# Kernel tuning notes

Hardware: AMD Instinct MI355X
Metric: run time of the kernel (lower is better)

## Reference

```python
import jax, jax.numpy as jnp
import numpy as np

N_NODES = 50000
N_EDGES = 800000
FEAT_DIM = 1024
EMBED_DIM = 128


def setup_inputs() -> dict:
    key = jax.random.key(0)
    k_x, k_w, k_r, k_c, k_v = jax.random.split(key, 5)
    x = jax.random.normal(k_x, (N_NODES, FEAT_DIM), dtype=jnp.float32)
    # xavier-uniform equivalent for weight [embed_dim, feat_dim]
    limit = float(np.sqrt(6.0 / (EMBED_DIM + FEAT_DIM)))
    weight = jax.random.uniform(k_w, (EMBED_DIM, FEAT_DIM), dtype=jnp.float32,
                                minval=-limit, maxval=limit)
    # sparse adjacency in COO form (row = destination, col = source)
    adj_row = jax.random.randint(k_r, (N_EDGES,), 0, N_NODES, dtype=jnp.int32)
    adj_col = jax.random.randint(k_c, (N_EDGES,), 0, N_NODES, dtype=jnp.int32)
    adj_vals = jax.random.uniform(k_v, (N_EDGES,), dtype=jnp.float32)
    return {"x": x, "weight": weight, "adj_row": adj_row,
            "adj_col": adj_col, "adj_vals": adj_vals}


def reference(x, weight, adj_row, adj_col, adj_vals):
    # Fused GeMM-SpMM: out = A @ (x @ W^T)
    h = jnp.einsum('nf,ef->ne', x, weight)          # [N, embed_dim] dense GEMM
    msgs = adj_vals[:, None] * h[adj_col]           # gather source rows, scale by edge weight
    out = jax.ops.segment_sum(msgs, adj_row, num_segments=N_NODES)  # scatter-add to dest rows
    return out
```

## Files before the change

kernel.cpp:

```cpp
#include <hip/hip_runtime.h>
#include <hip/hip_bf16.h>

#define FEAT 1024
#define EMBED 128
#define CAP 64
#define OVF_CAP 4096

#define NCH 16
#define A_BYTES 32768
#define B_BYTES 16384
#define BUF_BYTES 49152
#define NBUF 3

typedef __attribute__((ext_vector_type(8))) short short8;
typedef __attribute__((ext_vector_type(4))) float floatx4;

__device__ inline ushort f2bf(float f) {
    __hip_bfloat16 h = __float2bfloat16(f);
    return *reinterpret_cast<ushort*>(&h);
}
__device__ inline float bfbits_lo(uint u) {
    uint v = u << 16; return *reinterpret_cast<float*>(&v);
}
__device__ inline float bfbits_hi(uint u) {
    uint v = u & 0xffff0000u; return *reinterpret_cast<float*>(&v);
}

__device__ inline void async_copy16(const void* g, void* l) {
    __builtin_amdgcn_global_load_lds(
        (const __attribute__((address_space(1))) void*)g,
        (__attribute__((address_space(3))) void*)l, 16, 0, 0);
}

__global__ void swizzle_weight_kernel(const float* __restrict__ w,
                                      ushort* __restrict__ wbs) {
    int gid = blockIdx.x * blockDim.x + threadIdx.x;
    int l = gid & 63;
    int t = (gid >> 6) & 7;
    int s = gid >> 9;
    int row = t * 16 + (l & 15);
    int col = s * 32 + (l >> 4) * 8;
    const float* src = w + (size_t)row * FEAT + col;
    float4 v0 = *(const float4*)(src);
    float4 v1 = *(const float4*)(src + 4);
    short8 o;
    o[0] = f2bf(v0.x); o[1] = f2bf(v0.y); o[2] = f2bf(v0.z); o[3] = f2bf(v0.w);
    o[4] = f2bf(v1.x); o[5] = f2bf(v1.y); o[6] = f2bf(v1.z); o[7] = f2bf(v1.w);
    *(short8*)(wbs + (size_t)gid * 8) = o;
}

__launch_bounds__(256, 1)
__global__ void gemm_bucket_kernel(const float* __restrict__ x,
                                   const ushort* __restrict__ wbs,
                                   ushort* __restrict__ hb, int n_nodes,
                                   const int* __restrict__ adj_row,
                                   const int* __restrict__ adj_col,
                                   const float* __restrict__ adj_vals,
                                   int* __restrict__ cnt,
                                   int2* __restrict__ bucket,
                                   int* __restrict__ ovf_cnt,
                                   int* __restrict__ ovf_list,
                                   int n_edges, int gemm_blocks, int bucket_blocks) {
    __shared__ __align__(16) char lds[NBUF * BUF_BYTES];

    if (blockIdx.x >= gemm_blocks) {
        int stride = bucket_blocks * 256;
        for (int e = (blockIdx.x - gemm_blocks) * 256 + threadIdx.x;
             e < n_edges; e += stride) {
            int r = adj_row[e];
            int slot = atomicAdd(&cnt[r], 1);
            if (slot < CAP) {
                bucket[(size_t)r * CAP + slot] =
                    make_int2(adj_col[e], __float_as_int(adj_vals[e]));
            } else {
                int oi = atomicAdd(ovf_cnt, 1);
                if (oi < OVF_CAP) ovf_list[oi] = e;
            }
        }
        return;
    }

    const int lane = threadIdx.x & 63;
    const int wave = threadIdx.x >> 6;
    const int q    = lane >> 4;
    const int m    = lane & 15;
    const int base = blockIdx.x * 128 + wave * 32;
    const char* xb  = (const char*)x;
    const char* wbb = (const char*)wbs;

    size_t aoff[8];
#pragma unroll
    for (int k = 0; k < 8; ++k) {
        int r   = k * 4 + (lane >> 4);
        int row = base + r;
        if (row >= n_nodes) row = n_nodes - 1;
        int j = (lane & 15) ^ (r & 7);
        aoff[k] = (size_t)row * (FEAT * 4) + (size_t)j * 16;
    }

#define STAGE(c_) do {                                                        \
        char* buf_ = lds + ((c_) % NBUF) * BUF_BYTES;                         \
        char* Aw_  = buf_ + wave * 8192;                                      \
        _Pragma("unroll")                                                     \
        for (int k = 0; k < 8; ++k)                                           \
            async_copy16(xb + aoff[k] + (size_t)(c_) * 256, Aw_ + k * 1024);  \
        const char* bs_ = wbb + (size_t)(c_) * B_BYTES + wave * 1024 + lane * 16; \
        char* Bd_ = buf_ + A_BYTES + wave * 1024;                             \
        _Pragma("unroll")                                                     \
        for (int k = 0; k < 4; ++k)                                           \
            async_copy16(bs_ + k * 4096, Bd_ + k * 4096);                     \
    } while (0)

    STAGE(0); STAGE(1); STAGE(2);

    floatx4 acc[2][8];
#pragma unroll
    for (int rf = 0; rf < 2; ++rf)
#pragma unroll
        for (int t = 0; t < 8; ++t) acc[rf][t] = (floatx4)(0.0f);

    const int sw = (m & 7);
    for (int c = 0; c < NCH; ++c) {
        if (c <= NCH - 3)      asm volatile("s_waitcnt vmcnt(24)" ::: "memory");
        else if (c == NCH - 2) asm volatile("s_waitcnt vmcnt(12)" ::: "memory");
        else                   asm volatile("s_waitcnt vmcnt(0)"  ::: "memory");
        __builtin_amdgcn_sched_barrier(0);
        __builtin_amdgcn_s_barrier();
        __builtin_amdgcn_sched_barrier(0);

        const char* buf = lds + (c % NBUF) * BUF_BYTES;
        const char* Aw  = buf + wave * 8192;
        const char* Bb  = buf + A_BYTES;
#pragma unroll
        for (int s01 = 0; s01 < 2; ++s01) {
            int slot0 = s01 * 8 + q * 2;
            float4 a0l = *(const float4*)(Aw + m * 256 + ((slot0     ^ sw) * 16));
            float4 a0h = *(const float4*)(Aw + m * 256 + (((slot0+1) ^ sw) * 16));
            float4 a1l = *(const float4*)(Aw + (m+16) * 256 + ((slot0     ^ sw) * 16));
            float4 a1h = *(const float4*)(Aw + (m+16) * 256 + (((slot0+1) ^ sw) * 16));

            const char* bsrc = Bb + s01 * 8192 + lane * 16;
            short8 bf[8];
#pragma unroll
            for (int t = 0; t < 8; ++t) bf[t] = *(const short8*)(bsrc + t * 1024);

            short8 af0, af1;
            af0[0] = f2bf(a0l.x); af0[1] = f2bf(a0l.y);
            af0[2] = f2bf(a0l.z); af0[3] = f2bf(a0l.w);
            af0[4] = f2bf(a0h.x); af0[5] = f2bf(a0h.y);
            af0[6] = f2bf(a0h.z); af0[7] = f2bf(a0h.w);
            af1[0] = f2bf(a1l.x); af1[1] = f2bf(a1l.y);
            af1[2] = f2bf(a1l.z); af1[3] = f2bf(a1l.w);
            af1[4] = f2bf(a1h.x); af1[5] = f2bf(a1h.y);
            af1[6] = f2bf(a1h.z); af1[7] = f2bf(a1h.w);

#pragma unroll
            for (int t = 0; t < 8; ++t) {
                acc[0][t] = __builtin_amdgcn_mfma_f32_16x16x32_bf16(af0, bf[t], acc[0][t], 0, 0, 0);
                acc[1][t] = __builtin_amdgcn_mfma_f32_16x16x32_bf16(af1, bf[t], acc[1][t], 0, 0, 0);
            }
        }

        __builtin_amdgcn_s_barrier();
        __builtin_amdgcn_sched_barrier(0);
        if (c <= NCH - 4) STAGE(c + 3);
    }
#undef STAGE

#pragma unroll
    for (int rf = 0; rf < 2; ++rf) {
#pragma unroll
        for (int t = 0; t < 8; ++t) {
#pragma unroll
            for (int r = 0; r < 4; ++r) {
                int rr = base + rf * 16 + q * 4 + r;
                if (rr < n_nodes)
                    hb[(size_t)rr * EMBED + t * 16 + m] = f2bf(acc[rf][t][r]);
            }
        }
    }
}

__launch_bounds__(256)
__global__ void gather_kernel(const int* __restrict__ cnt,
                              const int2* __restrict__ bucket,
                              const ushort* __restrict__ hb,
                              const int* __restrict__ ovf_cnt,
                              const int* __restrict__ ovf_list,
                              const int* __restrict__ adj_row,
                              const int* __restrict__ adj_col,
                              const float* __restrict__ adj_vals,
                              float* __restrict__ out, int n_nodes) {
    int node = __builtin_amdgcn_readfirstlane(blockIdx.x * 4 + (threadIdx.x >> 6));
    if (node >= n_nodes) return;
    int lane = threadIdx.x & 63;
    int c_raw = cnt[node];
    int c = c_raw > CAP ? CAP : c_raw;
    const int2* bp = bucket + (size_t)node * CAP;
    const ushort* hl = hb + lane * 2;

    float accx = 0.0f, accy = 0.0f;
    int nb = c >> 4;
    if (nb > 0) {
        int4 eb[8];
#pragma unroll
        for (int i = 0; i < 8; ++i) eb[i] = *(const int4*)(bp + i * 2);
        for (int b = 0; b < nb; ++b) {
            uint u[16]; float wv[16];
#pragma unroll
            for (int i = 0; i < 8; ++i) {
                u[2*i]   = *(const uint*)(hl + (size_t)eb[i].x * EMBED);
                u[2*i+1] = *(const uint*)(hl + (size_t)eb[i].z * EMBED);
                wv[2*i]   = __int_as_float(eb[i].y);
                wv[2*i+1] = __int_as_float(eb[i].w);
            }
            if (b + 1 < nb) {
#pragma unroll
                for (int i = 0; i < 8; ++i)
                    eb[i] = *(const int4*)(bp + (b + 1) * 16 + i * 2);
            }
#pragma unroll
            for (int i = 0; i < 16; ++i) {
                accx = fmaf(wv[i], bfbits_lo(u[i]), accx);
                accy = fmaf(wv[i], bfbits_hi(u[i]), accy);
            }
        }
    }
    int j = nb * 16;
    for (; j + 2 <= c; j += 2) {
        int4 e01 = *(const int4*)(bp + j);
        uint u0 = *(const uint*)(hl + (size_t)e01.x * EMBED);
        uint u1 = *(const uint*)(hl + (size_t)e01.z * EMBED);
        float w0 = __int_as_float(e01.y), w1 = __int_as_float(e01.w);
        accx = fmaf(w0, bfbits_lo(u0), accx);  accy = fmaf(w0, bfbits_hi(u0), accy);
        accx = fmaf(w1, bfbits_lo(u1), accx);  accy = fmaf(w1, bfbits_hi(u1), accy);
    }
    if (j < c) {
        int2 ev = bp[j];
        uint u = *(const uint*)(hl + (size_t)ev.x * EMBED);
        float w = __int_as_float(ev.y);
        accx = fmaf(w, bfbits_lo(u), accx);
        accy = fmaf(w, bfbits_hi(u), accy);
    }
    if (c_raw > CAP) {
        int n = *ovf_cnt;
        if (n > OVF_CAP) n = OVF_CAP;
        for (int i = 0; i < n; ++i) {
            int e = ovf_list[i];
            if (adj_row[e] == node) {
                uint u = *(const uint*)(hl + (size_t)adj_col[e] * EMBED);
                float w = adj_vals[e];
                accx = fmaf(w, bfbits_lo(u), accx);
                accy = fmaf(w, bfbits_hi(u), accy);
            }
        }
    }
    *(float2*)(out + (size_t)node * EMBED + lane * 2) = make_float2(accx, accy);
}

extern "C" void kernel_launch(void* const* d_in, const int* in_sizes, int n_in,
                              void* d_out, int out_size, void* d_ws, size_t ws_size,
                              hipStream_t stream) {
    const float* x        = (const float*)d_in[0];
    const float* w        = (const float*)d_in[1];
    const int*   adj_row  = (const int*)d_in[2];
    const int*   adj_col  = (const int*)d_in[3];
    const float* adj_vals = (const float*)d_in[4];

    const int n_nodes = in_sizes[0] / FEAT;
    const int n_edges = in_sizes[2];
    float* out = (float*)d_out;

    char* ws = (char*)d_ws;
    ushort* wbs = (ushort*)ws;
    size_t off = 262144;
    ushort* hb = (ushort*)(ws + off);
    off += (size_t)n_nodes * EMBED * sizeof(ushort);
    char* meta = ws + off;
    int* cnt      = (int*)meta;
    int* ovf_cnt  = (int*)(meta + (size_t)n_nodes * 4);
    int* ovf_list = ovf_cnt + 1;
    size_t meta_bytes = ((size_t)n_nodes * 4 + 4 + OVF_CAP * 4 + 15) & ~(size_t)15;
    int2* bucket = (int2*)(meta + meta_bytes);

    hipMemsetAsync(meta, 0, meta_bytes, stream);

    swizzle_weight_kernel<<<64, 256, 0, stream>>>(w, wbs);

    const int gemm_blocks   = (n_nodes + 127) / 128;
    const int bucket_blocks = 512;
    gemm_bucket_kernel<<<gemm_blocks + bucket_blocks, 256, 0, stream>>>(
        x, wbs, hb, n_nodes,
        adj_row, adj_col, adj_vals,
        cnt, bucket, ovf_cnt, ovf_list, n_edges, gemm_blocks, bucket_blocks);

    gather_kernel<<<(n_nodes + 3) / 4, 256, 0, stream>>>(
        cnt, bucket, hb, ovf_cnt, ovf_list, adj_row, adj_col, adj_vals,
        out, n_nodes);
}
```

Baseline: 385.4 us.

## Load GEMM A operand directly to registers, shrink tiles, raise occupancy

Rewrites the GEMM portion so each wave computes 16 rows instead of 32. The x operand is loaded straight from global memory into registers with a one-chunk register prefetch, and only the bf16 weight chunks are double-buffered in LDS. LDS drops from 144 KB to 32 KB and launch bounds request 3 blocks per CU, aiming to overlap memory latency through occupancy rather than a deep async pipeline. It also doubles the bucketing blocks and adds an 8-edge unrolled tail in the gather kernel. The trade-off is that the weight B tile is reused across half as many rows, and the direct global loads of x are less coalesced than the old swizzled LDS staging.

```diff
diff --git a/kernel.cpp b/kernel.cpp
--- a/kernel.cpp
+++ b/kernel.cpp
@@ -6,11 +6,8 @@
 #define CAP 64
 #define OVF_CAP 4096
 
-#define NCH 16
-#define A_BYTES 32768
-#define B_BYTES 16384
-#define BUF_BYTES 49152
-#define NBUF 3
+#define NCHUNK 16
+#define B_CHUNK 16384
 
 typedef __attribute__((ext_vector_type(8))) short short8;
 typedef __attribute__((ext_vector_type(4))) float floatx4;
@@ -49,7 +46,7 @@
     *(short8*)(wbs + (size_t)gid * 8) = o;
 }
 
-__launch_bounds__(256, 1)
+__launch_bounds__(256, 3)
 __global__ void gemm_bucket_kernel(const float* __restrict__ x,
                                    const ushort* __restrict__ wbs,
                                    ushort* __restrict__ hb, int n_nodes,
@@ -61,7 +58,7 @@
                                    int* __restrict__ ovf_cnt,
                                    int* __restrict__ ovf_list,
                                    int n_edges, int gemm_blocks, int bucket_blocks) {
-    __shared__ __align__(16) char lds[NBUF * BUF_BYTES];
+    __shared__ __align__(16) char lds[2][B_CHUNK];
 
     if (blockIdx.x >= gemm_blocks) {
         int stride = bucket_blocks * 256;
@@ -84,99 +81,77 @@
     const int wave = threadIdx.x >> 6;
     const int q    = lane >> 4;
     const int m    = lane & 15;
-    const int base = blockIdx.x * 128 + wave * 32;
-    const char* xb  = (const char*)x;
+    const int base = blockIdx.x * 64 + wave * 16;
+
+    int row = base + m;
+    if (row >= n_nodes) row = n_nodes - 1;
+    const float* xp = x + (size_t)row * FEAT + q * 8;
     const char* wbb = (const char*)wbs;
 
-    size_t aoff[8];
-#pragma unroll
-    for (int k = 0; k < 8; ++k) {
-        int r   = k * 4 + (lane >> 4);
-        int row = base + r;
-        if (row >= n_nodes) row = n_nodes - 1;
-        int j = (lane & 15) ^ (r & 7);
-        aoff[k] = (size_t)row * (FEAT * 4) + (size_t)j * 16;
-    }
-
-#define STAGE(c_) do {                                                        \
-        char* buf_ = lds + ((c_) % NBUF) * BUF_BYTES;                         \
-        char* Aw_  = buf_ + wave * 8192;                                      \
-        _Pragma("unroll")                                                     \
-        for (int k = 0; k < 8; ++k)                                           \
-            async_copy16(xb + aoff[k] + (size_t)(c_) * 256, Aw_ + k * 1024);  \
-        const char* bs_ = wbb + (size_t)(c_) * B_BYTES + wave * 1024 + lane * 16; \
-        char* Bd_ = buf_ + A_BYTES + wave * 1024;                             \
-        _Pragma("unroll")                                                     \
-        for (int k = 0; k < 4; ++k)                                           \
-            async_copy16(bs_ + k * 4096, Bd_ + k * 4096);                     \
-    } while (0)
-
-    STAGE(0); STAGE(1); STAGE(2);
-
-    floatx4 acc[2][8];
-#pragma unroll
-    for (int rf = 0; rf < 2; ++rf)
-#pragma unroll
-        for (int t = 0; t < 8; ++t) acc[rf][t] = (floatx4)(0.0f);
-
-    const int sw = (m & 7);
-    for (int c = 0; c < NCH; ++c) {
-        if (c <= NCH - 3)      asm volatile("s_waitcnt vmcnt(24)" ::: "memory");
-        else if (c == NCH - 2) asm volatile("s_waitcnt vmcnt(12)" ::: "memory");
-        else                   asm volatile("s_waitcnt vmcnt(0)"  ::: "memory");
-        __builtin_amdgcn_sched_barrier(0);
-        __builtin_amdgcn_s_barrier();
-        __builtin_amdgcn_sched_barrier(0);
-
-        const char* buf = lds + (c % NBUF) * BUF_BYTES;
-        const char* Aw  = buf + wave * 8192;
-        const char* Bb  = buf + A_BYTES;
-#pragma unroll
-        for (int s01 = 0; s01 < 2; ++s01) {
-            int slot0 = s01 * 8 + q * 2;
-            float4 a0l = *(const float4*)(Aw + m * 256 + ((slot0     ^ sw) * 16));
-            float4 a0h = *(const float4*)(Aw + m * 256 + (((slot0+1) ^ sw) * 16));
-            float4 a1l = *(const float4*)(Aw + (m+16) * 256 + ((slot0     ^ sw) * 16));
-            float4 a1h = *(const float4*)(Aw + (m+16) * 256 + (((slot0+1) ^ sw) * 16));
-
-            const char* bsrc = Bb + s01 * 8192 + lane * 16;
+    {
+        const char* bs = wbb + wave * 4096 + lane * 16;
+        char* bd = lds[0] + wave * 4096;
+#pragma unroll
+        for (int k = 0; k < 4; ++k)
+            async_copy16(bs + k * 1024, bd + k * 1024);
+    }
+
+    float4 A0 = *(const float4*)(xp);
+    float4 A1 = *(const float4*)(xp + 4);
+    float4 A2 = *(const float4*)(xp + 32);
+    float4 A3 = *(const float4*)(xp + 36);
+
+    floatx4 acc[8];
+#pragma unroll
+    for (int t = 0; t < 8; ++t) acc[t] = (floatx4)(0.0f);
+
+    __syncthreads();
+
+    for (int c = 0; c < NCHUNK; ++c) {
+        const char* buf = lds[c & 1];
+        float4 N0, N1, N2, N3;
+        if (c + 1 < NCHUNK) {
+            const char* bs = wbb + (size_t)(c + 1) * B_CHUNK + wave * 4096 + lane * 16;
+            char* bd = lds[(c + 1) & 1] + wave * 4096;
+#pragma unroll
+            for (int k = 0; k < 4; ++k)
+                async_copy16(bs + k * 1024, bd + k * 1024);
+            const float* np = xp + (c + 1) * 64;
+            N0 = *(const float4*)(np);
+            N1 = *(const float4*)(np + 4);
+            N2 = *(const float4*)(np + 32);
+            N3 = *(const float4*)(np + 36);
+        }
+#pragma unroll
+        for (int sl = 0; sl < 2; ++sl) {
+            const char* bsrc = buf + sl * 8192 + lane * 16;
             short8 bf[8];
 #pragma unroll
             for (int t = 0; t < 8; ++t) bf[t] = *(const short8*)(bsrc + t * 1024);
 
-            short8 af0, af1;
-            af0[0] = f2bf(a0l.x); af0[1] = f2bf(a0l.y);
-            af0[2] = f2bf(a0l.z); af0[3] = f2bf(a0l.w);
-            af0[4] = f2bf(a0h.x); af0[5] = f2bf(a0h.y);
-            af0[6] = f2bf(a0h.z); af0[7] = f2bf(a0h.w);
-            af1[0] = f2bf(a1l.x); af1[1] = f2bf(a1l.y);
-            af1[2] = f2bf(a1l.z); af1[3] = f2bf(a1l.w);
-            af1[4] = f2bf(a1h.x); af1[5] = f2bf(a1h.y);
-            af1[6] = f2bf(a1h.z); af1[7] = f2bf(a1h.w);
-
-#pragma unroll
-            for (int t = 0; t < 8; ++t) {
-                acc[0][t] = __builtin_amdgcn_mfma_f32_16x16x32_bf16(af0, bf[t], acc[0][t], 0, 0, 0);
-                acc[1][t] = __builtin_amdgcn_mfma_f32_16x16x32_bf16(af1, bf[t], acc[1][t], 0, 0, 0);
-            }
-        }
-
-        __builtin_amdgcn_s_barrier();
-        __builtin_amdgcn_sched_barrier(0);
-        if (c <= NCH - 4) STAGE(c + 3);
-    }
-#undef STAGE
-
-#pragma unroll
-    for (int rf = 0; rf < 2; ++rf) {
-#pragma unroll
-        for (int t = 0; t < 8; ++t) {
-#pragma unroll
-            for (int r = 0; r < 4; ++r) {
-                int rr = base + rf * 16 + q * 4 + r;
-                if (rr < n_nodes)
-                    hb[(size_t)rr * EMBED + t * 16 + m] = f2bf(acc[rf][t][r]);
-            }
+            float4 al = sl ? A2 : A0;
+            float4 ah = sl ? A3 : A1;
+            short8 af;
+            af[0] = f2bf(al.x); af[1] = f2bf(al.y);
+            af[2] = f2bf(al.z); af[3] = f2bf(al.w);
+            af[4] = f2bf(ah.x); af[5] = f2bf(ah.y);
+            af[6] = f2bf(ah.z); af[7] = f2bf(ah.w);
+
+#pragma unroll
+            for (int t = 0; t < 8; ++t)
+                acc[t] = __builtin_amdgcn_mfma_f32_16x16x32_bf16(af, bf[t], acc[t], 0, 0, 0);
+        }
+        __syncthreads();
+        A0 = N0; A1 = N1; A2 = N2; A3 = N3;
+    }
+
+#pragma unroll
+    for (int t = 0; t < 8; ++t) {
+#pragma unroll
+        for (int r = 0; r < 4; ++r) {
+            int rr = base + q * 4 + r;
+            if (rr < n_nodes)
+                hb[(size_t)rr * EMBED + t * 16 + m] = f2bf(acc[t][r]);
         }
     }
 }
@@ -227,6 +202,25 @@
         }
     }
     int j = nb * 16;
+    if (j + 8 <= c) {
+        int4 eb[4];
+#pragma unroll
+        for (int i = 0; i < 4; ++i) eb[i] = *(const int4*)(bp + j + i * 2);
+        uint u[8]; float wv[8];
+#pragma unroll
+        for (int i = 0; i < 4; ++i) {
+            u[2*i]   = *(const uint*)(hl + (size_t)eb[i].x * EMBED);
+            u[2*i+1] = *(const uint*)(hl + (size_t)eb[i].z * EMBED);
+            wv[2*i]   = __int_as_float(eb[i].y);
+            wv[2*i+1] = __int_as_float(eb[i].w);
+        }
+#pragma unroll
+        for (int i = 0; i < 8; ++i) {
+            accx = fmaf(wv[i], bfbits_lo(u[i]), accx);
+            accy = fmaf(wv[i], bfbits_hi(u[i]), accy);
+        }
+        j += 8;
+    }
     for (; j + 2 <= c; j += 2) {
         int4 e01 = *(const int4*)(bp + j);
         uint u0 = *(const uint*)(hl + (size_t)e01.x * EMBED);
@@ -287,8 +281,8 @@
 
     swizzle_weight_kernel<<<64, 256, 0, stream>>>(w, wbs);
 
-    const int gemm_blocks   = (n_nodes + 127) / 128;
-    const int bucket_blocks = 512;
+    const int gemm_blocks   = (n_nodes + 63) / 64;
+    const int bucket_blocks = 1024;
     gemm_bucket_kernel<<<gemm_blocks + bucket_blocks, 256, 0, stream>>>(
         x, wbs, hb, n_nodes,
         adj_row, adj_col, adj_vals,
```

After: 365.1 us. -5.3%, faster.
